# Optimization experiments

Measured on AMD Instinct MI355X. Metric: run time of the kernel, lower is better.

## Reference

```python
import jax, jax.numpy as jnp
import numpy as np

B, T, D, V, LMAX = 16, 512, 256, 4233, 64
NEG = -1e30  # finite 'log zero' keeps grads NaN-free


def setup_inputs() -> dict:
    key = jax.random.key(0)
    k1, k2, k3, k4 = jax.random.split(key, 4)
    hs_pad = jax.random.normal(k1, (B, T, D), dtype=jnp.float32)
    hlens = jnp.full((B,), T, dtype=jnp.int32)
    ys_pad = jax.random.randint(k2, (B, LMAX), 1, V, dtype=jnp.int32)  # blank=0 excluded
    ys_lens = jax.random.randint(k3, (B,), LMAX // 2, LMAX + 1, dtype=jnp.int32)
    W = jax.random.normal(k4, (V, D), dtype=jnp.float32) * (1.0 / np.sqrt(D))
    b = jnp.zeros((V,), dtype=jnp.float32)
    return {"hs_pad": hs_pad, "hlens": hlens, "ys_pad": ys_pad,
            "ys_lens": ys_lens, "W": W, "b": b}


def _ctc_loss_sum(logp_tbv, ext, allow, hlens, ys_lens):
    """logp_tbv: [T,B,V] log-softmax; ext: [B,S] extended labels (blank-interleaved).
    Returns sum over batch of -log p(y|x) (torch CTCLoss reduction='sum')."""
    Tn, Bn, _ = logp_tbv.shape
    S = ext.shape[1]
    # per-frame log-prob of each extended label: [T,B,S]
    lp_ext = jnp.take_along_axis(
        logp_tbv, jnp.broadcast_to(ext[None], (Tn, Bn, S)), axis=2)

    # t = 0 init: alpha[0]=lp(blank), alpha[1]=lp(y_1)
    alpha0 = jnp.full((Bn, S), NEG, dtype=logp_tbv.dtype)
    alpha0 = alpha0.at[:, 0].set(lp_ext[0, :, 0])
    alpha0 = alpha0.at[:, 1].set(lp_ext[0, :, 1])

    def step(alpha, inp):
        lp_t, t = inp  # lp_t: [B,S]
        a1 = jnp.pad(alpha[:, :-1], ((0, 0), (1, 0)), constant_values=NEG)
        a2 = jnp.pad(alpha[:, :-2], ((0, 0), (2, 0)), constant_values=NEG)
        a2 = jnp.where(allow, a2, NEG)
        new = jnp.logaddexp(jnp.logaddexp(alpha, a1), a2) + lp_t
        alpha = jnp.where((t < hlens)[:, None], new, alpha)  # freeze past hlen
        return alpha, None

    ts = jnp.arange(1, Tn, dtype=jnp.int32)
    alpha, _ = jax.lax.scan(step, alpha0, (lp_ext[1:], ts))

    last = 2 * ys_lens  # index of final blank state
    bi = jnp.arange(Bn)
    ll = jnp.logaddexp(alpha[bi, last], alpha[bi, last - 1])
    return -jnp.sum(ll)


def reference(hs_pad, hlens, ys_pad, ys_lens, W, b):
    # linear projection + log_softmax (dropout_rate=0.0 -> identity)
    logits = jnp.einsum('btd,vd->btv', hs_pad, W) + b
    logp = jax.nn.log_softmax(logits, axis=-1)          # [B,T,V]
    logp = jnp.transpose(logp, (1, 0, 2))               # [T,B,V]

    Bn, Lmax = ys_pad.shape
    S = 2 * Lmax + 1
    ext = jnp.zeros((Bn, S), dtype=ys_pad.dtype).at[:, 1::2].set(ys_pad)
    prev2 = jnp.pad(ext, ((0, 0), (2, 0)))[:, :-2]
    allow = (ext != 0) & (ext != prev2) & (jnp.arange(S) >= 2)

    loss = _ctc_loss_sum(logp, ext, allow, hlens, ys_lens)
    return loss / Bn  # module divides by ys_hat.size(1) == batch
```

## Files before the change

kernel.cpp:

```cpp
#include <hip/hip_runtime.h>

constexpr int Bn = 16;
constexpr int Tn = 512;
constexpr int Dn = 256;
constexpr int Vn = 4233;
constexpr int Vp = 4352;
constexpr int Ln = 64;
constexpr int Un = 80;
constexpr int CS = 68;
constexpr int NCB = 34;
constexpr int Mtot = Bn * Tn;

#define LN2     0.6931471805599453f
#define INV_LN2 1.4426950408889634f

typedef __attribute__((ext_vector_type(8))) short short8;
typedef __attribute__((ext_vector_type(4))) float f32x4;

__device__ __forceinline__ float lg2(float x) { return __builtin_amdgcn_logf(x); }
__device__ __forceinline__ float ex2(float x) { return __builtin_amdgcn_exp2f(x); }

__device__ __forceinline__ unsigned short cvt_bf16(float f) {
    unsigned int u = __float_as_uint(f);
    u = (u + 0x7fffu + ((u >> 16) & 1u)) >> 16;
    return (unsigned short)u;
}

__device__ __forceinline__ void gl_lds16(const void* g, void* l) {
    __builtin_amdgcn_global_load_lds(
        (const __attribute__((address_space(1))) void*)g,
        (__attribute__((address_space(3))) void*)l,
        16, 0, 0);
}

__device__ __forceinline__ double dpp_shr1_d(double v) {
    union { double d; int i[2]; } u, r;
    u.d = v;
    r.i[0] = __builtin_amdgcn_update_dpp(0, u.i[0], 0x138, 0xF, 0xF, false);
    r.i[1] = __builtin_amdgcn_update_dpp(0, u.i[1], 0x138, 0xF, 0xF, false);
    return r.d;
}

__device__ __forceinline__ int wave_imax(int v) {
    int t;
    t = __builtin_amdgcn_update_dpp(v, v, 0xB1,  0xF, 0xF, false); v = (t > v) ? t : v;
    t = __builtin_amdgcn_update_dpp(v, v, 0x4E,  0xF, 0xF, false); v = (t > v) ? t : v;
    t = __builtin_amdgcn_update_dpp(v, v, 0x141, 0xF, 0xF, false); v = (t > v) ? t : v;
    t = __builtin_amdgcn_update_dpp(v, v, 0x140, 0xF, 0xF, false); v = (t > v) ? t : v;
    int a = __builtin_amdgcn_readlane(v, 0);
    int b = __builtin_amdgcn_readlane(v, 16);
    int c = __builtin_amdgcn_readlane(v, 32);
    int d = __builtin_amdgcn_readlane(v, 48);
    int ab = (a > b) ? a : b;
    int cd = (c > d) ? c : d;
    return (ab > cd) ? ab : cd;
}

__global__ __launch_bounds__(256) void conv(
    const float* __restrict__ hs, const float* __restrict__ W,
    const float* __restrict__ bias, const int* __restrict__ ys,
    unsigned short* __restrict__ hs_b, unsigned short* __restrict__ w_b,
    float* __restrict__ gbias, float* __restrict__ out)
{
    const int gid = blockIdx.x * 256 + threadIdx.x;
    const int stride = gridDim.x * 256;
    const float4* hs4 = (const float4*)hs;
    const float4* W4  = (const float4*)W;

    if (gid == 0) out[0] = 0.0f;

    for (int i = gid; i < (Bn * Tn * Dn) / 4; i += stride) {
        float4 v = hs4[i];
        ushort4 o = make_ushort4(cvt_bf16(v.x), cvt_bf16(v.y), cvt_bf16(v.z), cvt_bf16(v.w));
        *(ushort4*)(&hs_b[i * 4]) = o;
    }
    for (int i = gid; i < Vp * (Dn / 4); i += stride) {
        int row = i >> 6;
        float4 v = make_float4(0.f, 0.f, 0.f, 0.f);
        if (row < Vn) v = W4[i];
        ushort4 o = make_ushort4(cvt_bf16(v.x), cvt_bf16(v.y), cvt_bf16(v.z), cvt_bf16(v.w));
        *(ushort4*)(&w_b[i * 4]) = o;
    }
    for (int i = gid; i < Bn * 128; i += stride) {
        int b = i >> 7;
        int u = i & 127;
        int v = (u == 0) ? 0 : ((u <= Ln) ? ys[b * Ln + u - 1] : -1);
        gbias[i] = (v >= 0) ? bias[v] : 0.0f;
    }
}

__global__ __launch_bounds__(256) void gemm_se(
    const unsigned short* __restrict__ hs_b, const unsigned short* __restrict__ w_b,
    const int* __restrict__ ys, const float* __restrict__ bias,
    const float* __restrict__ gbias, float* __restrict__ sep,
    float* __restrict__ glg2)
{
    __shared__ __align__(16) short lsA[128 * 64];
    __shared__ __align__(16) short lsB[128 * 64];

    const int tid = threadIdx.x;
    const int lane = tid & 63;
    const int w = tid >> 6;
    const int lr = lane & 15;
    const int kq = lane >> 4;
    const int m0 = blockIdx.x * 128;
    const int mw = w * 32;
    const bool gather = (blockIdx.y == NCB);
    const int b = blockIdx.x >> 2;

    const int srow = lane >> 3;
    const int scg  = (lane & 7) ^ (srow & 7);
    const int scol = scg * 8;

    const unsigned short* bptr[4];
    #pragma unroll
    for (int j = 0; j < 4; ++j) {
        int c = w * 4 + j;
        int row = c * 8 + srow;
        int v;
        if (gather) {
            if (row == 0) v = 0;
            else if (row <= Ln) v = ys[b * Ln + row - 1];
            else v = Vn + 32;
        } else {
            v = blockIdx.y * 128 + row;
        }
        bptr[j] = w_b + (size_t)v * Dn + scol;
    }

    f32x4 acc[2][8];
    #pragma unroll
    for (int mf = 0; mf < 2; ++mf)
        #pragma unroll
        for (int nf = 0; nf < 8; ++nf)
            acc[mf][nf] = (f32x4){0.f, 0.f, 0.f, 0.f};

    for (int ks = 0; ks < 4; ++ks) {
        const int k0 = ks * 64;
        __syncthreads();
        #pragma unroll
        for (int j = 0; j < 4; ++j) {
            int c = w * 4 + j;
            int row = c * 8 + srow;
            gl_lds16(hs_b + (size_t)(m0 + row) * Dn + k0 + scol, (char*)lsA + c * 1024);
            gl_lds16(bptr[j] + k0,                               (char*)lsB + c * 1024);
        }
        __syncthreads();

        #pragma unroll
        for (int sub = 0; sub < 2; ++sub) {
            short8 af[2], bf[8];
            #pragma unroll
            for (int mf = 0; mf < 2; ++mf) {
                int row = mw + mf * 16 + lr;
                int cg = (sub * 4 + kq) ^ (row & 7);
                af[mf] = *(const short8*)(&lsA[row * 64 + cg * 8]);
            }
            #pragma unroll
            for (int nf = 0; nf < 8; ++nf) {
                int row = nf * 16 + lr;
                int cg = (sub * 4 + kq) ^ (row & 7);
                bf[nf] = *(const short8*)(&lsB[row * 64 + cg * 8]);
            }
            #pragma unroll
            for (int mf = 0; mf < 2; ++mf)
                #pragma unroll
                for (int nf = 0; nf < 8; ++nf)
                    acc[mf][nf] = __builtin_amdgcn_mfma_f32_16x16x32_bf16(
                        af[mf], bf[nf], acc[mf][nf], 0, 0, 0);
        }
    }

    if (!gather) {
        const int n0 = blockIdx.y * 128;
        float bcol[8]; bool valid[8];
        #pragma unroll
        for (int nf = 0; nf < 8; ++nf) {
            int col = n0 + nf * 16 + lr;
            valid[nf] = (col < Vn);
            bcol[nf] = valid[nf] ? bias[col] : 0.0f;
        }
        #pragma unroll
        for (int mf = 0; mf < 2; ++mf) {
            #pragma unroll
            for (int r = 0; r < 4; ++r) {
                float s = 0.0f;
                #pragma unroll
                for (int nf = 0; nf < 8; ++nf)
                    if (valid[nf]) s += __expf(acc[mf][nf][r] + bcol[nf]);
                #pragma unroll
                for (int off = 1; off < 16; off <<= 1) s += __shfl_xor(s, off, 64);
                if (lr == 0)
                    sep[(size_t)blockIdx.y * Mtot + m0 + mw + mf * 16 + kq * 4 + r] = s;
            }
        }
    } else {
        #pragma unroll
        for (int mf = 0; mf < 2; ++mf) {
            #pragma unroll
            for (int nf = 0; nf < 5; ++nf) {
                int u = nf * 16 + lr;
                float gv = gbias[b * 128 + u];
                #pragma unroll
                for (int r = 0; r < 4; ++r) {
                    int g = m0 + mw + mf * 16 + kq * 4 + r;
                    glg2[(size_t)g * Un + u] = (acc[mf][nf][r] + gv) * INV_LN2;
                }
            }
        }
    }
}

__global__ __launch_bounds__(256) void lse_norm(
    const float* __restrict__ sep, float* __restrict__ glg2)
{
    __shared__ float sl[64];
    const int tid = threadIdx.x;
    const int g0 = blockIdx.x * 64;

    if (tid < 64) {
        float s = 0.0f;
        #pragma unroll
        for (int c = 0; c < NCB; ++c) s += sep[(size_t)c * Mtot + g0 + tid];
        sl[tid] = lg2(s);
    }
    __syncthreads();

    #pragma unroll
    for (int j = 0; j < 4; ++j) {
        int i = tid + j * 256;
        int row = i >> 4, u4 = (i & 15) * 4;
        float* p = glg2 + (size_t)(g0 + row) * Un + u4;
        float4 v = *(const float4*)p;
        float sub = sl[row];
        v.x = ex2(v.x - sub); v.y = ex2(v.y - sub);
        v.z = ex2(v.z - sub); v.w = ex2(v.w - sub);
        *(float4*)p = v;
    }
    if (tid < 64) {
        float* p = glg2 + (size_t)(g0 + tid) * Un + 64;
        *p = ex2(*p - sl[tid]);
    }
}

__global__ __launch_bounds__(256) void ctc_fwd(
    const float* __restrict__ pmat, const int* __restrict__ ys,
    const int* __restrict__ hlens, const int* __restrict__ ylens,
    float* __restrict__ out)
{
    __shared__ float ls[2][64 * CS + 4];
    __shared__ double shO[64], shE[64], shZ[64];
    __shared__ int   shX[64];

    const int b = blockIdx.x;
    const int tid = threadIdx.x;
    const int l = tid & 63;

    const int hl = hlens[b];
    int yl  = ys[b * Ln + l];
    int ylm = (l >= 1) ? ys[b * Ln + l - 1] : -1;
    const double aF = ((l >= 1) && (yl != ylm)) ? 1.0 : 0.0;

    const float* pm = pmat + (size_t)b * Tn * Un;

    #pragma unroll
    for (int j = 0; j < 4; ++j) {
        int i = tid + j * 256;
        int tt = i >> 4, u4 = (i & 15) * 4;
        *(float4*)(&ls[0][tt * CS + u4]) = *(const float4*)(pm + (size_t)(1 + tt) * Un + u4);
    }
    if (tid < 64) ls[0][tid * CS + 64] = pm[(size_t)(1 + tid) * Un + 64];
    __syncthreads();

    double o = (l == 0) ? (double)pm[1] : 0.0;
    double e = (l == 0) ? (double)pm[0] : 0.0;
    double z = 0.0;
    int ex = 0;

    float4 r4a = make_float4(0.f,0.f,0.f,0.f), r4b = r4a, r4c = r4a, r4d = r4a;
    float r1 = 0.0f;

    double qa0, qa1, qa2, qa3, ra0, ra1, ra2, ra3;
    double qb0, qb1, qb2, qb3, rb0, rb1, rb2, rb3;
    double qc0, qc1, qc2, qc3, rc0, rc1, rc2, rc3;

#define RENORM32 do { \
        double mm = fmax(fmax(o, e), z); \
        union { double d; unsigned int ui[2]; } um; um.d = mm; \
        int kk = (int)((um.ui[1] >> 20) & 2047u) - 1023; \
        int km = wave_imax(kk); \
        o = ldexp(o, -km); e = ldexp(e, -km); z = ldexp(z, -km); \
        ex += km; \
    } while (0)

#define STEPR(qv, rv) do { \
        double an = dpp_shr1_d(o); \
        double nO = fma(aF, an, o + e) * (rv); \
        double nE = (e + an) * (qv); \
        double nZ = (z + o) * (qv); \
        o = nO; e = nE; z = nZ; \
    } while (0)

#define LDA(base) do { \
        qa0 = (double)buf[(base) * CS];       ra0 = (double)buf[(base) * CS + 1 + l]; \
        qa1 = (double)buf[((base)+1) * CS];   ra1 = (double)buf[((base)+1) * CS + 1 + l]; \
        qa2 = (double)buf[((base)+2) * CS];   ra2 = (double)buf[((base)+2) * CS + 1 + l]; \
        qa3 = (double)buf[((base)+3) * CS];   ra3 = (double)buf[((base)+3) * CS + 1 + l]; \
    } while (0)
#define LDB(base) do { \
        qb0 = (double)buf[(base) * CS];       rb0 = (double)buf[(base) * CS + 1 + l]; \
        qb1 = (double)buf[((base)+1) * CS];   rb1 = (double)buf[((base)+1) * CS + 1 + l]; \
        qb2 = (double)buf[((base)+2) * CS];   rb2 = (double)buf[((base)+2) * CS + 1 + l]; \
        qb3 = (double)buf[((base)+3) * CS];   rb3 = (double)buf[((base)+3) * CS + 1 + l]; \
    } while (0)
#define LDC(base) do { \
        qc0 = (double)buf[(base) * CS];       rc0 = (double)buf[(base) * CS + 1 + l]; \
        qc1 = (double)buf[((base)+1) * CS];   rc1 = (double)buf[((base)+1) * CS + 1 + l]; \
        qc2 = (double)buf[((base)+2) * CS];   rc2 = (double)buf[((base)+2) * CS + 1 + l]; \
        qc3 = (double)buf[((base)+3) * CS];   rc3 = (double)buf[((base)+3) * CS + 1 + l]; \
    } while (0)

#define W4A do { STEPR(qa0,ra0); STEPR(qa1,ra1); STEPR(qa2,ra2); STEPR(qa3,ra3); } while (0)
#define W4B do { STEPR(qb0,rb0); STEPR(qb1,rb1); STEPR(qb2,rb2); STEPR(qb3,rb3); } while (0)
#define W4C do { STEPR(qc0,rc0); STEPR(qc1,rc1); STEPR(qc2,rc2); STEPR(qc3,rc3); } while (0)

#define STEPS(Joff, ACT) do { \
        RENORM32; \
        double q = (double)buf[(Joff) * CS]; \
        double r = (double)buf[(Joff) * CS + 1 + l]; \
        double an = dpp_shr1_d(o); \
        double nO = fma(aF, an, o + e) * r; \
        double nE = (e + an) * q; \
        double nZ = (z + o) * q; \
        bool act = (ACT); \
        o = act ? nO : o; e = act ? nE : e; z = act ? nZ : z; \
    } while (0)

    for (int c = 0; c < 8; ++c) {
        if (c < 7) {
            const int tb = 1 + (c + 1) * 64;
            { int i = tid;       int tt = i >> 4, u4 = (i & 15) * 4;
              r4a = (tb + tt < Tn) ? *(const float4*)(pm + (size_t)(tb + tt) * Un + u4) : make_float4(0.f,0.f,0.f,0.f); }
            { int i = tid + 256; int tt = i >> 4, u4 = (i & 15) * 4;
              r4b = (tb + tt < Tn) ? *(const float4*)(pm + (size_t)(tb + tt) * Un + u4) : make_float4(0.f,0.f,0.f,0.f); }
            { int i = tid + 512; int tt = i >> 4, u4 = (i & 15) * 4;
              r4c = (tb + tt < Tn) ? *(const float4*)(pm + (size_t)(tb + tt) * Un + u4) : make_float4(0.f,0.f,0.f,0.f); }
            { int i = tid + 768; int tt = i >> 4, u4 = (i & 15) * 4;
              r4d = (tb + tt < Tn) ? *(const float4*)(pm + (size_t)(tb + tt) * Un + u4) : make_float4(0.f,0.f,0.f,0.f); }
            if (tid < 64)
                r1 = (tb + tid < Tn) ? pm[(size_t)(tb + tid) * Un + 64] : 0.0f;
        }

        const float* buf = ls[c & 1];

        if (c < 7) {
            if (hl >= (c + 1) * 64 + 1) {
                RENORM32;
                LDA(0); LDB(4);
                LDC(8);  W4A;
                LDA(12); W4B;
                LDB(16); W4C;
                LDC(20); W4A;
                LDA(24); W4B;
                LDB(28); W4C;
                LDC(32); W4A;
                LDA(36); W4B;
                RENORM32;
                LDB(40); W4C;
                LDC(44); W4A;
                LDA(48); W4B;
                LDB(52); W4C;
                LDC(56); W4A;
                LDA(60); W4B;
                W4C;
                W4A;
            } else {
                #pragma unroll 1
                for (int j = 0; j < 64; ++j)
                    STEPS(j, (c * 64 + 1 + j) < hl);
            }
        } else {
            if (hl >= Tn) {
                RENORM32;
                LDA(0); LDB(4);
                LDC(8);  W4A;
                LDA(12); W4B;
                LDB(16); W4C;
                LDC(20); W4A;
                LDA(24); W4B;
                LDB(28); W4C;
                LDC(32); W4A;
                LDA(36); W4B;
                RENORM32;
                LDB(40); W4C;
                LDC(44); W4A;
                LDA(48); W4B;
                LDB(52); W4C;
                LDC(56); W4A;
                LDA(60); W4B;
                W4C;
                STEPR(qa0, ra0); STEPR(qa1, ra1); STEPR(qa2, ra2);
            } else {
                #pragma unroll 1
                for (int j = 0; j < 63; ++j)
                    STEPS(j, (449 + j) < hl);
            }
        }

        if (c < 7) {
            float* dst = ls[(c + 1) & 1];
            { int i = tid;       int tt = i >> 4, u4 = (i & 15) * 4; *(float4*)(&dst[tt * CS + u4]) = r4a; }
            { int i = tid + 256; int tt = i >> 4, u4 = (i & 15) * 4; *(float4*)(&dst[tt * CS + u4]) = r4b; }
            { int i = tid + 512; int tt = i >> 4, u4 = (i & 15) * 4; *(float4*)(&dst[tt * CS + u4]) = r4c; }
            { int i = tid + 768; int tt = i >> 4, u4 = (i & 15) * 4; *(float4*)(&dst[tt * CS + u4]) = r4d; }
            if (tid < 64) dst[tid * CS + 64] = r1;
        }
        __syncthreads();
    }
#undef RENORM32
#undef STEPR
#undef LDA
#undef LDB
#undef LDC
#undef W4A
#undef W4B
#undef W4C
#undef STEPS

    if (tid < 64) { shO[l] = o; shE[l] = e; shZ[l] = z; shX[l] = ex; }
    __syncthreads();

    if (tid == 0) {
        int L = ylens[b];
        double vo = shO[L - 1]; int xo = shX[L - 1];
        double ve; int xe;
        if (L == 64) { ve = shZ[63]; xe = shX[63]; }
        else         { ve = shE[L];  xe = shX[L]; }
        int em = (xo > xe) ? xo : xe;
        double s = ldexp(vo, xo - em) + ldexp(ve, xe - em);
        union { double d; unsigned int ui[2]; } us; us.d = s;
        int ks = (int)((us.ui[1] >> 20) & 2047u) - 1023;
        double mant = ldexp(s, -ks);
        float ll = (lg2((float)mant) + (float)(ks + em)) * LN2;
        atomicAdd(out, -ll / (float)Bn);
    }
}

extern "C" void kernel_launch(void* const* d_in, const int* in_sizes, int n_in,
                              void* d_out, int out_size, void* d_ws, size_t ws_size,
                              hipStream_t stream) {
    const float* hs    = (const float*)d_in[0];
    const int*   hlens = (const int*)d_in[1];
    const int*   ys    = (const int*)d_in[2];
    const int*   ylens = (const int*)d_in[3];
    const float* W     = (const float*)d_in[4];
    const float* bias  = (const float*)d_in[5];
    float* out = (float*)d_out;

    char* ws = (char*)d_ws;
    unsigned short* hs_b = (unsigned short*)(ws);
    unsigned short* w_b  = (unsigned short*)(ws + 4194304);
    float* glg2  = (float*)(ws + 6422528);
    float* sep   = (float*)(ws + 9043968);
    float* gbias = (float*)(ws + 10158080);

    conv<<<1024, 256, 0, stream>>>(hs, W, bias, ys, hs_b, w_b, gbias, out);
    gemm_se<<<dim3(64, NCB + 1), 256, 0, stream>>>(hs_b, w_b, ys, bias, gbias, sep, glg2);
    lse_norm<<<Mtot / 64, 256, 0, stream>>>(sep, glg2);
    ctc_fwd<<<Bn, 256, 0, stream>>>(glg2, ys, hlens, ylens, out);
}
```

Baseline: 121.1 us.

## Fold log-sum-exp normalization into CTC kernel as additive loss correction

Removes the separate lse_norm kernel. The CTC recursion now runs on unnormalized probabilities: ex2 of the raw log2 logits is applied when tiles are staged into shared memory. The per-frame log-normalizer is added to the loss as a constant correction, computed by 16 extra blocks that reduce the sep partial sums over valid frames. This saves one launch and a full read-modify-write pass over glg2, at the cost of extra exponentials in the CTC load path and reliance on the existing per-wave renormalization to keep unnormalized values in range.

```diff
diff --git a/kernel.cpp b/kernel.cpp
--- a/kernel.cpp
+++ b/kernel.cpp
@@ -211,51 +211,48 @@
     }
 }
 
-__global__ __launch_bounds__(256) void lse_norm(
-    const float* __restrict__ sep, float* __restrict__ glg2)
+__global__ __launch_bounds__(256) void ctc_fwd(
+    const float* __restrict__ pmat, const float* __restrict__ sep,
+    const int* __restrict__ ys, const int* __restrict__ hlens,
+    const int* __restrict__ ylens, float* __restrict__ out)
 {
-    __shared__ float sl[64];
-    const int tid = threadIdx.x;
-    const int g0 = blockIdx.x * 64;
-
-    if (tid < 64) {
-        float s = 0.0f;
-        #pragma unroll
-        for (int c = 0; c < NCB; ++c) s += sep[(size_t)c * Mtot + g0 + tid];
-        sl[tid] = lg2(s);
-    }
-    __syncthreads();
-
-    #pragma unroll
-    for (int j = 0; j < 4; ++j) {
-        int i = tid + j * 256;
-        int row = i >> 4, u4 = (i & 15) * 4;
-        float* p = glg2 + (size_t)(g0 + row) * Un + u4;
-        float4 v = *(const float4*)p;
-        float sub = sl[row];
-        v.x = ex2(v.x - sub); v.y = ex2(v.y - sub);
-        v.z = ex2(v.z - sub); v.w = ex2(v.w - sub);
-        *(float4*)p = v;
-    }
-    if (tid < 64) {
-        float* p = glg2 + (size_t)(g0 + tid) * Un + 64;
-        *p = ex2(*p - sl[tid]);
-    }
-}
-
-__global__ __launch_bounds__(256) void ctc_fwd(
-    const float* __restrict__ pmat, const int* __restrict__ ys,
-    const int* __restrict__ hlens, const int* __restrict__ ylens,
-    float* __restrict__ out)
-{
-    __shared__ float ls[2][64 * CS + 4];
-    __shared__ double shO[64], shE[64], shZ[64];
-    __shared__ int   shX[64];
-
-    const int b = blockIdx.x;
+    __shared__ __align__(16) union SMem {
+        struct {
+            float ls[2][64 * CS + 4];
+            double shO[64], shE[64], shZ[64];
+            int   shX[64];
+        } c;
+        struct { float wsum[4]; } r;
+    } sm;
+
     const int tid = threadIdx.x;
     const int l = tid & 63;
-
+    const int w = tid >> 6;
+
+    if (blockIdx.x >= 16) {
+        const int b = blockIdx.x - 16;
+        const int hl = hlens[b];
+        float corrAcc = 0.0f;
+        #pragma unroll
+        for (int j = 0; j < 2; ++j) {
+            int t = tid + j * 256;
+            float s = 0.0f;
+            #pragma unroll
+            for (int c = 0; c < NCB; ++c)
+                s += sep[(size_t)c * Mtot + b * Tn + t];
+            if (t < hl) corrAcc += lg2(s);
+        }
+        #pragma unroll
+        for (int off = 1; off < 64; off <<= 1) corrAcc += __shfl_xor(corrAcc, off, 64);
+        if (l == 0) sm.r.wsum[w] = corrAcc;
+        __syncthreads();
+        if (tid == 0)
+            atomicAdd(out, (sm.r.wsum[0] + sm.r.wsum[1] + sm.r.wsum[2] + sm.r.wsum[3])
+                           * (LN2 / (float)Bn));
+        return;
+    }
+
+    const int b = blockIdx.x;
     const int hl = hlens[b];
     int yl  = ys[b * Ln + l];
     int ylm = (l >= 1) ? ys[b * Ln + l - 1] : -1;
@@ -267,13 +264,15 @@
     for (int j = 0; j < 4; ++j) {
         int i = tid + j * 256;
         int tt = i >> 4, u4 = (i & 15) * 4;
-        *(float4*)(&ls[0][tt * CS + u4]) = *(const float4*)(pm + (size_t)(1 + tt) * Un + u4);
-    }
-    if (tid < 64) ls[0][tid * CS + 64] = pm[(size_t)(1 + tid) * Un + 64];
+        float4 v = *(const float4*)(pm + (size_t)(1 + tt) * Un + u4);
+        v.x = ex2(v.x); v.y = ex2(v.y); v.z = ex2(v.z); v.w = ex2(v.w);
+        *(float4*)(&sm.c.ls[0][tt * CS + u4]) = v;
+    }
+    if (tid < 64) sm.c.ls[0][tid * CS + 64] = ex2(pm[(size_t)(1 + tid) * Un + 64]);
     __syncthreads();
 
-    double o = (l == 0) ? (double)pm[1] : 0.0;
-    double e = (l == 0) ? (double)pm[0] : 0.0;
+    double o = (l == 0) ? (double)ex2(pm[1]) : 0.0;
+    double e = (l == 0) ? (double)ex2(pm[0]) : 0.0;
     double z = 0.0;
     int ex = 0;
 
@@ -351,7 +350,7 @@
                 r1 = (tb + tid < Tn) ? pm[(size_t)(tb + tid) * Un + 64] : 0.0f;
         }
 
-        const float* buf = ls[c & 1];
+        const float* buf = sm.c.ls[c & 1];
 
         if (c < 7) {
             if (hl >= (c + 1) * 64 + 1) {
@@ -408,12 +407,26 @@
         }
 
         if (c < 7) {
-            float* dst = ls[(c + 1) & 1];
-            { int i = tid;       int tt = i >> 4, u4 = (i & 15) * 4; *(float4*)(&dst[tt * CS + u4]) = r4a; }
-            { int i = tid + 256; int tt = i >> 4, u4 = (i & 15) * 4; *(float4*)(&dst[tt * CS + u4]) = r4b; }
-            { int i = tid + 512; int tt = i >> 4, u4 = (i & 15) * 4; *(float4*)(&dst[tt * CS + u4]) = r4c; }
-            { int i = tid + 768; int tt = i >> 4, u4 = (i & 15) * 4; *(float4*)(&dst[tt * CS + u4]) = r4d; }
-            if (tid < 64) dst[tid * CS + 64] = r1;
+            const int tb = 1 + (c + 1) * 64;
+            float* dst = sm.c.ls[(c + 1) & 1];
+            { int i = tid;       int tt = i >> 4, u4 = (i & 15) * 4; float4 v = r4a;
+              v.x = ex2(v.x); v.y = ex2(v.y); v.z = ex2(v.z); v.w = ex2(v.w);
+              if (tb + tt >= Tn) v = make_float4(0.f,0.f,0.f,0.f);
+              *(float4*)(&dst[tt * CS + u4]) = v; }
+            { int i = tid + 256; int tt = i >> 4, u4 = (i & 15) * 4; float4 v = r4b;
+              v.x = ex2(v.x); v.y = ex2(v.y); v.z = ex2(v.z); v.w = ex2(v.w);
+              if (tb + tt >= Tn) v = make_float4(0.f,0.f,0.f,0.f);
+              *(float4*)(&dst[tt * CS + u4]) = v; }
+            { int i = tid + 512; int tt = i >> 4, u4 = (i & 15) * 4; float4 v = r4c;
+              v.x = ex2(v.x); v.y = ex2(v.y); v.z = ex2(v.z); v.w = ex2(v.w);
+              if (tb + tt >= Tn) v = make_float4(0.f,0.f,0.f,0.f);
+              *(float4*)(&dst[tt * CS + u4]) = v; }
+            { int i = tid + 768; int tt = i >> 4, u4 = (i & 15) * 4; float4 v = r4d;
+              v.x = ex2(v.x); v.y = ex2(v.y); v.z = ex2(v.z); v.w = ex2(v.w);
+              if (tb + tt >= Tn) v = make_float4(0.f,0.f,0.f,0.f);
+              *(float4*)(&dst[tt * CS + u4]) = v; }
+            if (tid < 64)
+                dst[tid * CS + 64] = (tb + tid < Tn) ? ex2(r1) : 0.0f;
         }
         __syncthreads();
     }
@@ -427,15 +440,15 @@
 #undef W4C
 #undef STEPS
 
-    if (tid < 64) { shO[l] = o; shE[l] = e; shZ[l] = z; shX[l] = ex; }
+    if (tid < 64) { sm.c.shO[l] = o; sm.c.shE[l] = e; sm.c.shZ[l] = z; sm.c.shX[l] = ex; }
     __syncthreads();
 
     if (tid == 0) {
         int L = ylens[b];
-        double vo = shO[L - 1]; int xo = shX[L - 1];
+        double vo = sm.c.shO[L - 1]; int xo = sm.c.shX[L - 1];
         double ve; int xe;
-        if (L == 64) { ve = shZ[63]; xe = shX[63]; }
-        else         { ve = shE[L];  xe = shX[L]; }
+        if (L == 64) { ve = sm.c.shZ[63]; xe = sm.c.shX[63]; }
+        else         { ve = sm.c.shE[L];  xe = sm.c.shX[L]; }
         int em = (xo > xe) ? xo : xe;
         double s = ldexp(vo, xo - em) + ldexp(ve, xe - em);
         union { double d; unsigned int ui[2]; } us; us.d = s;
@@ -466,6 +479,5 @@
 
     conv<<<1024, 256, 0, stream>>>(hs, W, bias, ys, hs_b, w_b, gbias, out);
     gemm_se<<<dim3(64, NCB + 1), 256, 0, stream>>>(hs_b, w_b, ys, bias, gbias, sep, glg2);
-    lse_norm<<<Mtot / 64, 256, 0, stream>>>(sep, glg2);
-    ctc_fwd<<<Bn, 256, 0, stream>>>(glg2, ys, hlens, ylens, out);
-}
+    ctc_fwd<<<32, 256, 0, stream>>>(glg2, sep, ys, hlens, ylens, out);
+}
```

Measured after the change: 117.4 us. 1.03x faster.
